# Performance work log

Measured on AMD Instinct MI355X. Metric: run time of the kernel, lower is better.

Reference implementation:

```python
import jax, jax.numpy as jnp
import numpy as np

L, B, S, D, N, H = 4, 4, 1024, 1024, 64, 16   # layers, batch, seq, d_model, d_state, heads
DI = 2 * D      # d_inner (expand_factor=2)
DH = D // H     # head dim
DF = 4 * D      # ffn hidden
SCALE = 1.0 / np.sqrt(DH)


def setup_inputs() -> dict:
    key = jax.random.key(0)
    ks = jax.random.split(key, 12)
    w = lambda k, sh: jax.random.normal(k, sh, jnp.float32) * 0.02
    return {
        "x": jax.random.normal(ks[0], (B, S, D), jnp.float32),
        "A_log": jax.random.normal(ks[1], (L, N), jnp.float32),
        "Dp": jax.random.normal(ks[2], (L, D), jnp.float32),
        "W_in": w(ks[3], (L, 2 * DI, D)), "b_in": jnp.zeros((L, 2 * DI), jnp.float32),
        "W_xp": w(ks[4], (L, N, DI)), "b_xp": jnp.zeros((L, N), jnp.float32),
        "W_dt": w(ks[5], (L, D, DI)), "b_dt": jnp.zeros((L, D), jnp.float32),
        "W_out": w(ks[6], (L, D, DI)), "b_out": jnp.zeros((L, D), jnp.float32),
        "W_qkv": w(ks[7], (L, 3 * D, D)), "b_qkv": jnp.zeros((L, 3 * D), jnp.float32),
        "W_ao": w(ks[8], (L, D, D)), "b_ao": jnp.zeros((L, D), jnp.float32),
        "g1": jnp.ones((L, D), jnp.float32), "be1": jnp.zeros((L, D), jnp.float32),
        "g2": jnp.ones((L, D), jnp.float32), "be2": jnp.zeros((L, D), jnp.float32),
        "W_f1": w(ks[9], (L, DF, D)), "b_f1": jnp.zeros((L, DF), jnp.float32),
        "W_f2": w(ks[10], (L, D, DF)), "b_f2": jnp.zeros((L, D), jnp.float32),
    }


def _ln(x, g, b, eps=1e-5):
    mu = x.mean(-1, keepdims=True)
    var = ((x - mu) ** 2).mean(-1, keepdims=True)
    return (x - mu) * jax.lax.rsqrt(var + eps) * g + b


def _mamba(x, A_log, Dp, W_in, b_in, W_xp, b_xp, W_dt, b_dt, W_out, b_out):
    xr = jnp.einsum('bsd,od->bso', x, W_in) + b_in          # [b,s,2*DI]
    xi, res = jnp.split(xr, 2, axis=-1)
    xi = jax.nn.silu(xi)
    A = -jnp.exp(A_log)                                      # [N]
    delta = jax.nn.softplus(jnp.einsum('bsi,di->bsd', xi, W_dt) + b_dt)  # [b,s,D]
    m = delta.mean(-1)                                       # [b,s]
    A_disc = jnp.exp(A[None, None, :] * m[:, :, None])       # [b,s,N]
    u = jnp.einsum('bsi,ni->bsn', xi, W_xp) + b_xp           # [b,s,N]

    def step(state, inp):
        a_t, u_t = inp
        state = a_t * state + u_t                            # [b,N]
        return state, state.sum(-1)                          # carry, emit sum over d_state

    init = jnp.zeros((x.shape[0], A_log.shape[0]), x.dtype)
    _, ssum = jax.lax.scan(step, init, (A_disc.swapaxes(0, 1), u.swapaxes(0, 1)))
    ssum = ssum.swapaxes(0, 1)                               # [b,s]
    y = ssum[..., None] * xi                                 # [b,s,DI]
    y = y * jax.nn.silu(res)
    y = jnp.einsum('bsi,di->bsd', y, W_out) + b_out
    return y + x * Dp


def _attn(x, W_qkv, b_qkv, W_ao, b_ao):
    b, s, d = x.shape
    qkv = jnp.einsum('bsd,od->bso', x, W_qkv) + b_qkv        # [b,s,3d]
    qkv = qkv.reshape(b, s, 3, H, DH)
    q = jnp.moveaxis(qkv[:, :, 0], 2, 1)                     # [b,h,s,dh]
    k = jnp.moveaxis(qkv[:, :, 1], 2, 1)
    v = jnp.moveaxis(qkv[:, :, 2], 2, 1)
    scores = jnp.einsum('bhqd,bhkd->bhqk', q, k) * SCALE
    wts = jax.nn.softmax(scores, axis=-1)
    o = jnp.einsum('bhqk,bhkd->bhqd', wts, v)
    o = jnp.moveaxis(o, 1, 2).reshape(b, s, d)
    return jnp.einsum('bsd,od->bso', o, W_ao) + b_ao


def _forward(x, A_log, Dp, W_in, b_in, W_xp, b_xp, W_dt, b_dt, W_out, b_out,
             W_qkv, b_qkv, W_ao, b_ao, g1, be1, g2, be2, W_f1, b_f1, W_f2, b_f2):
    for l in range(L):
        m = _mamba(x, A_log[l], Dp[l], W_in[l], b_in[l], W_xp[l], b_xp[l],
                   W_dt[l], b_dt[l], W_out[l], b_out[l])
        x = _ln(x + m, g1[l], be1[l])
        a = _attn(x, W_qkv[l], b_qkv[l], W_ao[l], b_ao[l])
        x = _ln(x + a, g2[l], be2[l])
        h = jax.nn.gelu(jnp.einsum('bsd,fd->bsf', x, W_f1[l]) + b_f1[l], approximate=False)
        x = x + jnp.einsum('bsf,df->bsd', h, W_f2[l]) + b_f2[l]
    return x


def reference(x, A_log, Dp, W_in, b_in, W_xp, b_xp, W_dt, b_dt, W_out, b_out,
              W_qkv, b_qkv, W_ao, b_ao, g1, be1, g2, be2, W_f1, b_f1, W_f2, b_f2):
    return _forward(x, A_log, Dp, W_in, b_in, W_xp, b_xp, W_dt, b_dt, W_out, b_out,
                    W_qkv, b_qkv, W_ao, b_ao, g1, be1, g2, be2, W_f1, b_f1, W_f2, b_f2)
```

## Files before the change

### kernel.cpp

```cpp
#include <hip/hip_runtime.h>
#include <math.h>

typedef unsigned short ushort_t;
typedef unsigned int uint_t;
typedef __attribute__((ext_vector_type(8))) short short8;
typedef __attribute__((ext_vector_type(4))) float f32x4;

constexpr int Bb = 4, Ss = 1024, Dd = 1024, Nn = 64, Hh = 16;
constexpr int DIi = 2048, DFf = 4096;
constexpr int TOKENS = Bb * Ss;

constexpr size_t O_IN  = 0;
constexpr size_t O_DT  = 4194304;
constexpr size_t O_XP  = O_DT + 2097152;
constexpr size_t O_OUT = O_XP + 262144;
constexpr size_t O_QKV = O_OUT + 2097152;
constexpr size_t O_AO  = O_QKV + 3145728;
constexpr size_t O_F1  = O_AO + 1048576;
constexpr size_t O_F2  = O_F1 + 4194304;
constexpr size_t W_TOTAL = O_F2 + 4194304;
constexpr size_t W_QUADS = W_TOTAL / 4;

enum { EPI_SPLIT = 0, EPI_QKV, EPI_GELU, EPI_DTXP, EPI_DP, EPI_F32, EPI_RESID };

__device__ __forceinline__ float siluf(float x) { return x / (1.f + expf(-x)); }
__device__ __forceinline__ float softplusf(float x) { return fmaxf(x, 0.f) + log1pf(expf(-fabsf(x))); }
__device__ __forceinline__ float geluf(float x) { return 0.5f * x * (1.f + erff(x * 0.7071067811865476f)); }

__device__ __forceinline__ float bf2f(uint_t u) {
    union { uint_t i; float f; } v; v.i = u << 16; return v.f;
}
__device__ __forceinline__ ushort_t f2bf(float f) {
    union { float f; uint_t i; } v; v.f = f;
    return (ushort_t)((v.i + 0x7FFFu + ((v.i >> 16) & 1u)) >> 16);
}

__device__ __forceinline__ void gload_lds16(const ushort_t* g, ushort_t* l) {
    __builtin_amdgcn_global_load_lds(
        (const __attribute__((address_space(1))) unsigned int*)g,
        (__attribute__((address_space(3))) unsigned int*)l, 16, 0, 0);
}

__device__ __forceinline__ void wait_vm(int n) {
    if (n == 0)      asm volatile("s_waitcnt vmcnt(0)" ::: "memory");
    else if (n == 3) asm volatile("s_waitcnt vmcnt(3)" ::: "memory");
    else if (n == 4) asm volatile("s_waitcnt vmcnt(4)" ::: "memory");
    else if (n == 6) asm volatile("s_waitcnt vmcnt(6)" ::: "memory");
    else             asm volatile("s_waitcnt vmcnt(8)" ::: "memory");
}

template <int EPI>
__global__ __launch_bounds__(512) void gemm_mfma256(
    const ushort_t* __restrict__ A, const ushort_t* __restrict__ Bw,
    const float* __restrict__ bias, int M, int N, int K,
    ushort_t* __restrict__ ob0, ushort_t* __restrict__ ob1)
{
    constexpr int NBUF = 3, DEPTH = 2, L = 4;
    constexpr int BUFSZ = 16384;
    __shared__ __attribute__((aligned(16))) ushort_t AB[NBUF * BUFSZ];

    const int tid = threadIdx.x;
    const int lane = tid & 63, wid = tid >> 6;
    const int wr = wid >> 2, wc = wid & 3;
    const int l15 = lane & 15, lg = lane >> 4;

    int bx = blockIdx.x, by = blockIdx.y;
    const int gx = gridDim.x, gy = gridDim.y;
    if ((gy & 3) == 0 && (gx & 1) == 0) {
        const int s = by * gx + bx;
        const int xcd = s & 7, c = s >> 3;
        const int gyc = gy >> 2, gxc = gx >> 1;
        by = (xcd & 3) * gyc + (c % gyc);
        bx = (xcd >> 2) * gxc + (c / gyc);
    }
    const int m0 = by << 8, n0 = bx << 8;

    f32x4 acc[8][4];
#pragma unroll
    for (int i = 0; i < 8; ++i)
#pragma unroll
        for (int j = 0; j < 4; ++j) { acc[i][j][0]=0.f; acc[i][j][1]=0.f; acc[i][j][2]=0.f; acc[i][j][3]=0.f; }

    const int srow4 = lane >> 2;
    const int scc4  = (lane & 3) ^ ((lane >> 3) & 3);
    const ushort_t* Ag = A + (size_t)(m0 + wid * 32 + srow4) * K + scc4 * 8;
    const ushort_t* Bg = Bw + (size_t)(n0 + wid * 32 + srow4) * K + scc4 * 8;

    auto STAGE = [&](int b_, int k0_) {
        ushort_t* d_ = AB + b_ * BUFSZ;
        gload_lds16(Ag + k0_,                  d_ + (wid * 32) * 32);
        gload_lds16(Ag + (size_t)16 * K + k0_, d_ + (wid * 32 + 16) * 32);
        gload_lds16(Bg + k0_,                  d_ + 8192 + (wid * 32) * 32);
        gload_lds16(Bg + (size_t)16 * K + k0_, d_ + 8192 + (wid * 32 + 16) * 32);
    };

    const int NS = K >> 5;
    STAGE(0, 0);
    STAGE(1, 32);
    wait_vm(4);
    __builtin_amdgcn_s_barrier();

    const int chAB = (lg ^ ((l15 >> 1) & 3)) * 8;
    int bc = 0, bp = DEPTH;
    for (int s = 0; s < NS; ++s) {
        if (s + DEPTH < NS) STAGE(bp, (s + DEPTH) << 5);
        const ushort_t* As_ = AB + bc * BUFSZ;
        const ushort_t* Bs_ = As_ + 8192;
        short8 af[8], bfr[4];
#pragma unroll
        for (int mi = 0; mi < 8; ++mi)
            af[mi] = *(const short8*)&As_[(wr * 128 + mi * 16 + l15) * 32 + chAB];
#pragma unroll
        for (int nj = 0; nj < 4; ++nj)
            bfr[nj] = *(const short8*)&Bs_[(wc * 64 + nj * 16 + l15) * 32 + chAB];
#pragma unroll
        for (int mi = 0; mi < 8; ++mi)
#pragma unroll
            for (int nj = 0; nj < 4; ++nj)
                acc[mi][nj] = __builtin_amdgcn_mfma_f32_16x16x32_bf16(
                    af[mi], bfr[nj], acc[mi][nj], 0, 0, 0);
        if (s + 1 < NS) {
            wait_vm((s + 2 < NS) ? 4 : 0);
            __builtin_amdgcn_s_barrier();
        }
        bc = (bc + 1 == NBUF) ? 0 : bc + 1;
        bp = (bp + 1 == NBUF) ? 0 : bp + 1;
    }
    __syncthreads();

    const bool lo = (EPI != EPI_SPLIT) || (n0 < DIi);
#pragma unroll
    for (int pass = 0; pass < 2; ++pass) {
        if (pass) __syncthreads();
        if (wr == pass) {
#pragma unroll
            for (int nj = 0; nj < 4; ++nj) {
                const int coll = wc * 64 + nj * 16 + l15;
                const float bv = bias[n0 + coll];
#pragma unroll
                for (int mi = 0; mi < 8; ++mi)
#pragma unroll
                    for (int r = 0; r < 4; ++r) {
                        float v = acc[mi][nj][r] + bv;
                        if (EPI == EPI_SPLIT) v = lo ? siluf(v) : v;
                        else if (EPI == EPI_GELU) v = geluf(v);
                        AB[(mi * 16 + lg * 4 + r) * 256 + coll] = f2bf(v);
                    }
            }
        }
        __syncthreads();
        const int tok0 = m0 + pass * 128;
        if (EPI == EPI_QKV && n0 >= 2048) {
            const int bb = tok0 >> 10, srow0 = tok0 & 1023;
#pragma unroll
            for (int it = 0; it < 8; ++it) {
                const int task = it * 512 + tid;
                const int dim = task & 255;
                const int strip = task >> 8;
                uint_t w[4];
#pragma unroll
                for (int j = 0; j < 4; ++j) {
                    const int s2 = strip * 8 + 2 * j;
                    w[j] = (uint_t)AB[s2 * 256 + dim] | ((uint_t)AB[(s2 + 1) * 256 + dim] << 16);
                }
                const int vd = (n0 - 2048) + dim;
                *(uint4*)&ob1[((size_t)(bb * Hh + (vd >> 6)) * 64 + (vd & 63)) * Ss + srow0 + strip * 8] =
                    make_uint4(w[0], w[1], w[2], w[3]);
            }
        } else {
            ushort_t* dst = (EPI == EPI_SPLIT) ? (lo ? ob0 : ob1) : ob0;
            const int Nd = (EPI == EPI_SPLIT) ? DIi : N;
            const int nb = (EPI == EPI_SPLIT && !lo) ? (n0 - DIi) : n0;
#pragma unroll
            for (int it = 0; it < 8; ++it) {
                const int c = it * 512 + tid;
                const int row = c >> 5, ch = c & 31;
                *(uint4*)&dst[(size_t)(tok0 + row) * Nd + nb + ch * 8] =
                    *(const uint4*)&AB[row * 256 + ch * 8];
            }
        }
    }
}

template <int EPI, int MT, int NBUF, int XBY>
__global__ __launch_bounds__(256) void gemm_mfma(
    const ushort_t* __restrict__ A, const ushort_t* __restrict__ Bw,
    const float* __restrict__ bias, int M, int N, int K,
    float* __restrict__ of0, float* __restrict__ of1,
    ushort_t* __restrict__ ob0, ushort_t* __restrict__ ob1,
    const float* __restrict__ e0, const float* __restrict__ e1)
{
    constexpr int BUFSZ = (MT == 128) ? 8192 : 6144;
    constexpr int DEPTH = NBUF - 1;
    constexpr int L     = (MT == 128) ? 4 : 3;
    constexpr int NJ    = (MT == 128) ? 4 : 2;
    constexpr int XBX   = 8 / XBY;
    __shared__ __attribute__((aligned(16))) ushort_t AB[NBUF * BUFSZ];

    const int tid = threadIdx.x;
    const int lane = tid & 63, wid = tid >> 6;
    const int wr = (MT == 128) ? (wid >> 1) : 0;
    const int wc = (MT == 128) ? (wid & 1) : wid;
    const int l15 = lane & 15, lg = lane >> 4;

    int bx = blockIdx.x, by = blockIdx.y;
    const int gx = gridDim.x, gy = gridDim.y;
    if ((gy % XBY) == 0 && (gx % XBX) == 0) {
        const int s = by * gx + bx;
        const int xcd = s & 7, c = s >> 3;
        const int gyc = gy / XBY, gxc = gx / XBX;
        by = (xcd % XBY) * gyc + (c % gyc);
        bx = (xcd / XBY) * gxc + (c / gyc);
    }
    const int m0 = by * MT, n0 = bx << 7;

    f32x4 acc[4][NJ];
#pragma unroll
    for (int i = 0; i < 4; ++i)
#pragma unroll
        for (int j = 0; j < NJ; ++j) { acc[i][j][0] = 0.f; acc[i][j][1] = 0.f; acc[i][j][2] = 0.f; acc[i][j][3] = 0.f; }

    const int srow4 = lane >> 2;
    const int scc4  = (lane & 3) ^ ((lane >> 3) & 3);
    const ushort_t* Ag = A + (size_t)(m0 + wid * 32 + srow4) * K + scc4 * 8;
    const ushort_t* Bg = Bw + (size_t)(n0 + wid * 32 + srow4) * K + scc4 * 8;
    const ushort_t* sb64[3];
    int do64[3];
    if (MT == 64) {
#pragma unroll
        for (int j = 0; j < 3; ++j) {
            const int i = wid * 3 + j;
            const bool isA = i < 4;
            const int rb = (isA ? i : i - 4) * 16;
            sb64[j] = (isA ? A + (size_t)(m0 + rb + srow4) * K
                           : Bw + (size_t)(n0 + rb + srow4) * K) + scc4 * 8;
            do64[j] = (isA ? 0 : 2048) + rb * 32;
        }
    }

    auto STAGE = [&](int b_, int k0_) {
        ushort_t* d_ = AB + b_ * BUFSZ;
        if constexpr (MT == 128) {
            gload_lds16(Ag + k0_,                  d_ + (wid * 32) * 32);
            gload_lds16(Ag + (size_t)16 * K + k0_, d_ + (wid * 32 + 16) * 32);
            gload_lds16(Bg + k0_,                  d_ + 4096 + (wid * 32) * 32);
            gload_lds16(Bg + (size_t)16 * K + k0_, d_ + 4096 + (wid * 32 + 16) * 32);
        } else {
#pragma unroll
            for (int j = 0; j < 3; ++j)
                gload_lds16(sb64[j] + k0_, d_ + do64[j]);
        }
    };

    const int NS = K >> 5;
#pragma unroll
    for (int p = 0; p < DEPTH; ++p) STAGE(p, p * 32);
    wait_vm((DEPTH - 1) * L);
    __builtin_amdgcn_s_barrier();

    const int chAB = (lg ^ ((l15 >> 1) & 3)) * 8;
    int bc = 0, bp = DEPTH;
    for (int s = 0; s < NS; ++s) {
        if (s + DEPTH < NS) STAGE(bp, (s + DEPTH) << 5);
        const ushort_t* As_ = AB + bc * BUFSZ;
        const ushort_t* Bs_ = As_ + ((MT == 128) ? 4096 : 2048);
        short8 af[4], bfr[NJ];
#pragma unroll
        for (int mi = 0; mi < 4; ++mi)
            af[mi] = *(const short8*)&As_[(wr * 64 + mi * 16 + l15) * 32 + chAB];
#pragma unroll
        for (int nj = 0; nj < NJ; ++nj)
            bfr[nj] = *(const short8*)&Bs_[(wc * (MT == 128 ? 64 : 32) + nj * 16 + l15) * 32 + chAB];
#pragma unroll
        for (int mi = 0; mi < 4; ++mi)
#pragma unroll
            for (int nj = 0; nj < NJ; ++nj)
                acc[mi][nj] = __builtin_amdgcn_mfma_f32_16x16x32_bf16(
                    af[mi], bfr[nj], acc[mi][nj], 0, 0, 0);
        if (s + 1 < NS) {
            const int rem = NS - 2 - s;
            wait_vm(((rem < DEPTH - 1) ? rem : DEPTH - 1) * L);
            __builtin_amdgcn_s_barrier();
        }
        bc = (bc + 1 == NBUF) ? 0 : bc + 1;
        bp = (bp + 1 == NBUF) ? 0 : bp + 1;
    }
    __syncthreads();

    if constexpr (MT == 128) {
        const bool lo = true; (void)lo;
#pragma unroll
        for (int nj = 0; nj < 4; ++nj) {
            const int coll = wc * 64 + nj * 16 + l15;
            const float bv = bias[n0 + coll];
#pragma unroll
            for (int mi = 0; mi < 4; ++mi)
#pragma unroll
                for (int r = 0; r < 4; ++r)
                    AB[(wr * 64 + mi * 16 + lg * 4 + r) * 128 + coll] = f2bf(acc[mi][nj][r] + bv);
        }
        __syncthreads();
#pragma unroll
        for (int i = 0; i < 8; ++i) {
            const int c = i * 256 + tid;
            const int row = c >> 4, ch = c & 15;
            *(uint4*)&ob0[(size_t)(m0 + row) * N + n0 + ch * 8] =
                *(const uint4*)&AB[row * 128 + ch * 8];
        }
    } else {
        float* Cf = (float*)AB;
#pragma unroll
        for (int nj = 0; nj < NJ; ++nj) {
            const int coll = wc * 32 + nj * 16 + l15;
            const float bv = bias[n0 + coll];
#pragma unroll
            for (int mi = 0; mi < 4; ++mi)
#pragma unroll
                for (int r = 0; r < 4; ++r)
                    Cf[(mi * 16 + lg * 4 + r) * 128 + coll] = acc[mi][nj][r] + bv;
        }
        __syncthreads();
#pragma unroll
        for (int i = 0; i < 8; ++i) {
            const int c = i * 256 + tid;
            const int row = c >> 5, ch = c & 31;
            const int grow = m0 + row;
            const int gcol = n0 + ch * 4;
            float4 v = *(const float4*)&Cf[row * 128 + ch * 4];
            if (EPI == EPI_DTXP) {
                if (n0 < Dd) {
                    float ps = softplusf(v.x) + softplusf(v.y) + softplusf(v.z) + softplusf(v.w);
#pragma unroll
                    for (int off = 1; off < 32; off <<= 1) ps += __shfl_xor(ps, off);
                    if ((lane & 31) == 0)
                        of0[(size_t)grow * 8 + (n0 >> 7)] = ps;
                } else {
                    *(float4*)&of1[(size_t)grow * 128 + (gcol - Dd)] = v;
                }
            } else if (EPI == EPI_DP) {
                const float4 e = *(const float4*)&e0[(size_t)grow * N + gcol];
                const float4 d = *(const float4*)&e1[gcol];
                v.x = fmaf(e.x, d.x, v.x); v.y = fmaf(e.y, d.y, v.y);
                v.z = fmaf(e.z, d.z, v.z); v.w = fmaf(e.w, d.w, v.w);
                *(float4*)&of0[(size_t)grow * N + gcol] = v;
            } else if (EPI == EPI_F32) {
                *(float4*)&of0[(size_t)grow * N + gcol] = v;
            } else {
                const float4 e = *(const float4*)&e0[(size_t)grow * N + gcol];
                v.x += e.x; v.y += e.y; v.z += e.z; v.w += e.w;
                *(float4*)&of0[(size_t)grow * N + gcol] = v;
                uint2 w;
                w.x = (uint_t)f2bf(v.x) | ((uint_t)f2bf(v.y) << 16);
                w.y = (uint_t)f2bf(v.z) | ((uint_t)f2bf(v.w) << 16);
                *(uint2*)&ob0[(size_t)grow * N + gcol] = w;
            }
        }
    }
}

__global__ __launch_bounds__(256) void convert_weights_kernel(
    const float* __restrict__ Win, const float* __restrict__ Wdt,
    const float* __restrict__ Wxp, const float* __restrict__ Wout,
    const float* __restrict__ Wqkv, const float* __restrict__ Wao,
    const float* __restrict__ Wf1, const float* __restrict__ Wf2,
    const float* __restrict__ bdt, const float* __restrict__ bxp,
    ushort_t* __restrict__ dst, float* __restrict__ bcat)
{
    size_t q = (size_t)blockIdx.x * blockDim.x + threadIdx.x;
    if (q < 288) {
#pragma unroll
        for (int j = 0; j < 4; ++j) {
            const int e = (int)q * 4 + j;
            bcat[e] = (e < Dd) ? bdt[e] : ((e < Dd + Nn) ? bxp[e - Dd] : 0.f);
        }
    }
    const size_t stride = (size_t)gridDim.x * blockDim.x;
    for (; q < W_QUADS; q += stride) {
        const size_t e = q * 4;
        float4 v;
        if (e < O_DT)       v = *(const float4*)&Win[e - O_IN];
        else if (e < O_XP)  v = *(const float4*)&Wdt[e - O_DT];
        else if (e < O_OUT) {
            const size_t li = e - O_XP;
            const int row = (int)(li >> 11), colq = (int)(li & 2047);
            v = (row < Nn) ? *(const float4*)&Wxp[(size_t)row * DIi + colq]
                           : make_float4(0.f, 0.f, 0.f, 0.f);
        }
        else if (e < O_QKV) v = *(const float4*)&Wout[e - O_OUT];
        else if (e < O_AO)  v = *(const float4*)&Wqkv[e - O_QKV];
        else if (e < O_F1)  v = *(const float4*)&Wao[e - O_AO];
        else if (e < O_F2)  v = *(const float4*)&Wf1[e - O_F1];
        else                v = *(const float4*)&Wf2[e - O_F2];
        uint2 w;
        w.x = (uint_t)f2bf(v.x) | ((uint_t)f2bf(v.y) << 16);
        w.y = (uint_t)f2bf(v.z) | ((uint_t)f2bf(v.w) << 16);
        *(uint2*)&dst[e] = w;
    }
}

__global__ __launch_bounds__(256) void cvt_f32_bf16_kernel(
    const float* __restrict__ in, ushort_t* __restrict__ out)
{
    const size_t i4 = (size_t)blockIdx.x * blockDim.x + threadIdx.x;
    const float4 v = *(const float4*)&in[i4 * 4];
    uint2 w;
    w.x = (uint_t)f2bf(v.x) | ((uint_t)f2bf(v.y) << 16);
    w.y = (uint_t)f2bf(v.z) | ((uint_t)f2bf(v.w) << 16);
    *(uint2*)&out[i4 * 4] = w;
}

__global__ __launch_bounds__(256) void ln_residual_kernel(
    float* __restrict__ xio, const float* __restrict__ addin,
    const float* __restrict__ g, const float* __restrict__ be,
    ushort_t* __restrict__ xb)
{
    __shared__ float red[8];
    const int tid = threadIdx.x;
    const size_t base = (size_t)blockIdx.x * Dd;
    const float4 xv = *(const float4*)&xio[base + tid * 4];
    const float4 av = *(const float4*)&addin[base + tid * 4];
    float v[4] = {xv.x + av.x, xv.y + av.y, xv.z + av.z, xv.w + av.w};
    float s = v[0] + v[1] + v[2] + v[3];
    float s2 = v[0] * v[0] + v[1] * v[1] + v[2] * v[2] + v[3] * v[3];
#pragma unroll
    for (int off = 32; off; off >>= 1) { s += __shfl_xor(s, off); s2 += __shfl_xor(s2, off); }
    if ((tid & 63) == 0) { red[tid >> 6] = s; red[4 + (tid >> 6)] = s2; }
    __syncthreads();
    const float mu = (red[0] + red[1] + red[2] + red[3]) * (1.f / (float)Dd);
    const float var = (red[4] + red[5] + red[6] + red[7]) * (1.f / (float)Dd) - mu * mu;
    const float rstd = rsqrtf(var + 1e-5f);
    const float4 gv = *(const float4*)&g[tid * 4];
    const float4 bv = *(const float4*)&be[tid * 4];
    float o[4];
    o[0] = (v[0] - mu) * rstd * gv.x + bv.x;
    o[1] = (v[1] - mu) * rstd * gv.y + bv.y;
    o[2] = (v[2] - mu) * rstd * gv.z + bv.z;
    o[3] = (v[3] - mu) * rstd * gv.w + bv.w;
    *(float4*)&xio[base + tid * 4] = make_float4(o[0], o[1], o[2], o[3]);
    uint2 w;
    w.x = (uint_t)f2bf(o[0]) | ((uint_t)f2bf(o[1]) << 16);
    w.y = (uint_t)f2bf(o[2]) | ((uint_t)f2bf(o[3]) << 16);
    *(uint2*)&xb[base + tid * 4] = w;
}

__global__ __launch_bounds__(1024) void scan_fused_kernel(
    const float* __restrict__ A_log_l, const float* __restrict__ part,
    const float* __restrict__ u, float* __restrict__ ssum)
{
    __shared__ float Ps[16][64];
    __shared__ float Sl[16][64];
    __shared__ float Cs[16][64];
    __shared__ float Ms[16][64];
    const int b = blockIdx.x;
    const int tid = threadIdx.x;
    const int n = tid & 63, c = tid >> 6;
    const int t0 = b * Ss + c * 64;
    const float Aval = -expf(A_log_l[n]);

    {
        const float* pp = part + (size_t)(t0 + n) * 8;
        float ps = 0.f;
#pragma unroll
        for (int j = 0; j < 8; ++j) ps += pp[j];
        Ms[c][n] = ps * (1.f / 1024.f);
    }
    __syncthreads();

    float S = 0.f, msum = 0.f;
#pragma unroll 8
    for (int t = 0; t < 64; ++t) {
        const float mt = Ms[c][t];
        msum += mt;
        S = fmaf(expf(Aval * mt), S, u[(size_t)(t0 + t) * 128 + n]);
    }
    Ps[c][n] = expf(Aval * msum);
    Sl[c][n] = S;
    __syncthreads();

    if (c == 0) {
        float carry = 0.f;
#pragma unroll
        for (int cc = 0; cc < 16; ++cc) {
            Cs[cc][n] = carry;
            carry = fmaf(Ps[cc][n], carry, Sl[cc][n]);
        }
    }
    __syncthreads();

    float st = Cs[c][n];
#pragma unroll 4
    for (int t = 0; t < 64; ++t) {
        st = fmaf(expf(Aval * Ms[c][t]), st, u[(size_t)(t0 + t) * 128 + n]);
        float r = st;
#pragma unroll
        for (int off = 32; off; off >>= 1) r += __shfl_xor(r, off);
        if (n == 0) ssum[t0 + t] = r;
    }
}

__global__ __launch_bounds__(256) void y_gate_kernel(
    ushort_t* __restrict__ xi, const ushort_t* __restrict__ res,
    const float* __restrict__ ssum)
{
    const size_t i8 = (size_t)blockIdx.x * blockDim.x + threadIdx.x;
    const int t = (int)(i8 >> 8);
    const float sv = ssum[t];
    uint4 xw = *(const uint4*)&xi[i8 * 8];
    const uint4 rw = *(const uint4*)&res[i8 * 8];
    const uint_t xs[4] = {xw.x, xw.y, xw.z, xw.w};
    const uint_t rs[4] = {rw.x, rw.y, rw.z, rw.w};
    uint_t os[4];
#pragma unroll
    for (int j = 0; j < 4; ++j) {
        const float x0 = bf2f(xs[j] & 0xffffu), x1 = bf2f(xs[j] >> 16);
        const float r0 = bf2f(rs[j] & 0xffffu), r1 = bf2f(rs[j] >> 16);
        os[j] = (uint_t)f2bf(sv * x0 * siluf(r0)) | ((uint_t)f2bf(sv * x1 * siluf(r1)) << 16);
    }
    *(uint4*)&xi[i8 * 8] = make_uint4(os[0], os[1], os[2], os[3]);
}

__global__ __launch_bounds__(256) void attn_mfma_kernel(
    const ushort_t* __restrict__ qkv, const ushort_t* __restrict__ vt,
    ushort_t* __restrict__ out)
{
    __shared__ ushort_t Ks[64 * 64];
    __shared__ ushort_t Vs[64 * 64];
    __shared__ __attribute__((aligned(16))) ushort_t Pb[4][2560];

    const int tid = threadIdx.x;
    const int lane = tid & 63, wid = tid >> 6;
    const int b = blockIdx.z, h = blockIdx.y;
    const int q0 = blockIdx.x * 128 + wid * 32;
    const int l15 = lane & 15, lg = lane >> 4;
    constexpr float CEXP = 0.125f * 1.44269504f;

    short8 qf[2][2];
#pragma unroll
    for (int mi = 0; mi < 2; ++mi)
#pragma unroll
        for (int kk = 0; kk < 2; ++kk)
            qf[mi][kk] = *(const short8*)&qkv[(size_t)(b * Ss + q0 + mi * 16 + l15) * 3072
                                              + h * 64 + kk * 32 + lg * 8];

    f32x4 oacc[2][4];
#pragma unroll
    for (int mi = 0; mi < 2; ++mi)
#pragma unroll
        for (int nj = 0; nj < 4; ++nj) { oacc[mi][nj][0]=0.f; oacc[mi][nj][1]=0.f; oacc[mi][nj][2]=0.f; oacc[mi][nj][3]=0.f; }
    float lrun[2][4];
#pragma unroll
    for (int mi = 0; mi < 2; ++mi)
#pragma unroll
        for (int r = 0; r < 4; ++r) lrun[mi][r] = 0.f;

    const int srow = lane >> 3;
    const int scc  = (lane & 7) ^ srow;
    const ushort_t* Kg = qkv + (size_t)(b * Ss + wid * 16 + srow) * 3072 + 1024 + h * 64 + scc * 8;
    const ushort_t* Vg = vt + (size_t)((b * Hh + h) * 64 + wid * 16 + srow) * Ss + scc * 8;

    for (int kt = 0; kt < Ss / 64; ++kt) {
#pragma unroll
        for (int j = 0; j < 2; ++j) {
            gload_lds16(Kg + (size_t)(kt * 64 + j * 8) * 3072, Ks + (wid * 16 + j * 8) * 64);
            gload_lds16(Vg + (size_t)j * 8 * Ss + kt * 64,     Vs + (wid * 16 + j * 8) * 64);
        }
        __syncthreads();

        f32x4 sacc[2][4];
#pragma unroll
        for (int mi = 0; mi < 2; ++mi)
#pragma unroll
            for (int nj = 0; nj < 4; ++nj) { sacc[mi][nj][0]=0.f; sacc[mi][nj][1]=0.f; sacc[mi][nj][2]=0.f; sacc[mi][nj][3]=0.f; }
#pragma unroll
        for (int kk = 0; kk < 2; ++kk) {
            short8 kf[4];
#pragma unroll
            for (int nj = 0; nj < 4; ++nj) {
                const int row = nj * 16 + l15;
                const int ch = (kk * 4 + lg) ^ (row & 7);
                kf[nj] = *(const short8*)&Ks[row * 64 + ch * 8];
            }
#pragma unroll
            for (int mi = 0; mi < 2; ++mi)
#pragma unroll
                for (int nj = 0; nj < 4; ++nj)
                    sacc[mi][nj] = __builtin_amdgcn_mfma_f32_16x16x32_bf16(
                        qf[mi][kk], kf[nj], sacc[mi][nj], 0, 0, 0);
        }

#pragma unroll
        for (int mi = 0; mi < 2; ++mi)
#pragma unroll
            for (int nj = 0; nj < 4; ++nj) {
                const int bi = mi * 2 + (nj >> 1);
                const int chsw = ((nj & 1) * 2 + (l15 >> 3)) ^ lg;
#pragma unroll
                for (int r = 0; r < 4; ++r) {
                    const float p = exp2f(sacc[mi][nj][r] * CEXP);
                    lrun[mi][r] += p;
                    const int q15 = lg * 4 + r;
                    Pb[wid][bi * 640 + q15 * 40 + chsw * 8 + (lane & 7)] = f2bf(p);
                }
            }

#pragma unroll
        for (int kk = 0; kk < 2; ++kk) {
            short8 pa[2], vb[4];
#pragma unroll
            for (int mi = 0; mi < 2; ++mi) {
                const int chsw = lg ^ (l15 >> 2);
                pa[mi] = *(const short8*)&Pb[wid][(mi * 2 + kk) * 640 + l15 * 40 + chsw * 8];
            }
#pragma unroll
            for (int nj = 0; nj < 4; ++nj) {
                const int row = nj * 16 + l15;
                const int ch = (kk * 4 + lg) ^ (row & 7);
                vb[nj] = *(const short8*)&Vs[row * 64 + ch * 8];
            }
#pragma unroll
            for (int mi = 0; mi < 2; ++mi)
#pragma unroll
                for (int nj = 0; nj < 4; ++nj)
                    oacc[mi][nj] = __builtin_amdgcn_mfma_f32_16x16x32_bf16(
                        pa[mi], vb[nj], oacc[mi][nj], 0, 0, 0);
        }
        __syncthreads();
    }

#pragma unroll
    for (int mi = 0; mi < 2; ++mi)
#pragma unroll
        for (int r = 0; r < 4; ++r) {
            float s = lrun[mi][r];
#pragma unroll
            for (int off = 1; off < 16; off <<= 1) s += __shfl_xor(s, off);
            lrun[mi][r] = 1.f / s;
        }
#pragma unroll
    for (int mi = 0; mi < 2; ++mi)
#pragma unroll
        for (int r = 0; r < 4; ++r) {
            const int q = q0 + mi * 16 + lg * 4 + r;
            const float inv = lrun[mi][r];
#pragma unroll
            for (int nj = 0; nj < 4; ++nj)
                out[(size_t)(b * Ss + q) * Dd + h * 64 + nj * 16 + l15] =
                    f2bf(oacc[mi][nj][r] * inv);
        }
}

extern "C" void kernel_launch(void* const* d_in, const int* in_sizes, int n_in,
                              void* d_out, int out_size, void* d_ws, size_t ws_size,
                              hipStream_t stream)
{
    const float* x_in  = (const float*)d_in[0];
    const float* A_log = (const float*)d_in[1];
    const float* Dp    = (const float*)d_in[2];
    const float* W_in  = (const float*)d_in[3];
    const float* b_in  = (const float*)d_in[4];
    const float* W_xp  = (const float*)d_in[5];
    const float* b_xp  = (const float*)d_in[6];
    const float* W_dt  = (const float*)d_in[7];
    const float* b_dt  = (const float*)d_in[8];
    const float* W_out = (const float*)d_in[9];
    const float* b_out = (const float*)d_in[10];
    const float* W_qkv = (const float*)d_in[11];
    const float* b_qkv = (const float*)d_in[12];
    const float* W_ao  = (const float*)d_in[13];
    const float* b_ao  = (const float*)d_in[14];
    const float* g1    = (const float*)d_in[15];
    const float* be1   = (const float*)d_in[16];
    const float* g2    = (const float*)d_in[17];
    const float* be2   = (const float*)d_in[18];
    const float* W_f1  = (const float*)d_in[19];
    const float* b_f1  = (const float*)d_in[20];
    const float* W_f2  = (const float*)d_in[21];
    const float* b_f2  = (const float*)d_in[22];

    float* xf      = (float*)d_ws;
    float* a3      = xf + 4194304;
    float* ub      = a3 + 4194304;
    float* sb      = ub + 524288;
    float* part    = sb + 4096;
    float* bcat    = part + 32768;
    ushort_t* xb    = (ushort_t*)(bcat + 1152);
    ushort_t* xi_b  = xb + 4194304;
    ushort_t* res_b = xi_b + 8388608;
    ushort_t* qh_b  = res_b + 8388608;
    ushort_t* ao_b  = qh_b + 16777216;
    ushort_t* Wb    = ao_b + 4194304;
    ushort_t* vt_b  = Wb + W_TOTAL;

    hipMemcpyAsync(xf, x_in, (size_t)TOKENS * Dd * sizeof(float),
                   hipMemcpyDeviceToDevice, stream);
    cvt_f32_bf16_kernel<<<dim3(4096), dim3(256), 0, stream>>>(x_in, xb);

    const dim3 blk(256), blk512(512);

    for (int l = 0; l < 4; ++l) {
        convert_weights_kernel<<<dim3(2048), blk, 0, stream>>>(
            W_in + (size_t)l * 4194304, W_dt + (size_t)l * 2097152,
            W_xp + (size_t)l * 131072,  W_out + (size_t)l * 2097152,
            W_qkv + (size_t)l * 3145728, W_ao + (size_t)l * 1048576,
            W_f1 + (size_t)l * 4194304, W_f2 + (size_t)l * 4194304,
            b_dt + (size_t)l * 1024, b_xp + (size_t)l * Nn, Wb, bcat);

        gemm_mfma256<EPI_SPLIT><<<dim3(16, 16), blk512, 0, stream>>>(
            xb, Wb + O_IN, b_in + (size_t)l * 4096, TOKENS, 4096, 1024,
            xi_b, res_b);
        gemm_mfma<EPI_DTXP, 64, 4, 8><<<dim3(9, 64), blk, 0, stream>>>(
            xi_b, Wb + O_DT, bcat, TOKENS, 1152, 2048,
            part, ub, nullptr, nullptr, nullptr, nullptr);
        scan_fused_kernel<<<dim3(Bb), dim3(1024), 0, stream>>>(
            A_log + (size_t)l * Nn, part, ub, sb);
        y_gate_kernel<<<dim3(4096), blk, 0, stream>>>(xi_b, res_b, sb);
        gemm_mfma<EPI_DP, 64, 4, 8><<<dim3(8, 64), blk, 0, stream>>>(
            xi_b, Wb + O_OUT, b_out + (size_t)l * 1024, TOKENS, 1024, 2048,
            a3, nullptr, nullptr, nullptr, xf, Dp + (size_t)l * 1024);
        ln_residual_kernel<<<dim3(TOKENS), blk, 0, stream>>>(
            xf, a3, g1 + (size_t)l * 1024, be1 + (size_t)l * 1024, xb);
        gemm_mfma256<EPI_QKV><<<dim3(12, 16), blk512, 0, stream>>>(
            xb, Wb + O_QKV, b_qkv + (size_t)l * 3072, TOKENS, 3072, 1024,
            qh_b, vt_b);
        attn_mfma_kernel<<<dim3(8, Hh, Bb), blk, 0, stream>>>(qh_b, vt_b, ao_b);
        gemm_mfma<EPI_F32, 64, 4, 8><<<dim3(8, 64), blk, 0, stream>>>(
            ao_b, Wb + O_AO, b_ao + (size_t)l * 1024, TOKENS, 1024, 1024,
            a3, nullptr, nullptr, nullptr, nullptr, nullptr);
        ln_residual_kernel<<<dim3(TOKENS), blk, 0, stream>>>(
            xf, a3, g2 + (size_t)l * 1024, be2 + (size_t)l * 1024, xb);
        gemm_mfma256<EPI_GELU><<<dim3(16, 16), blk512, 0, stream>>>(
            xb, Wb + O_F1, b_f1 + (size_t)l * 4096, TOKENS, 4096, 1024,
            qh_b, nullptr);
        gemm_mfma<EPI_RESID, 64, 4, 8><<<dim3(8, 64), blk, 0, stream>>>(
            qh_b, Wb + O_F2, b_f2 + (size_t)l * 1024, TOKENS, 1024, 4096,
            xf, nullptr, xb, nullptr, xf, nullptr);
    }

    hipMemcpyAsync(d_out, xf, (size_t)TOKENS * Dd * sizeof(float),
                   hipMemcpyDeviceToDevice, stream);
    (void)in_sizes; (void)n_in; (void)out_size; (void)ws_size;
}
```

Measured before the change: 1.864 ms.

## Rework 256-wide GEMM to K=64 double buffering; move QKV to 128-tile GEMM

Rewrites the 256x256 GEMM kernel to stage K=64 slices with two buffers and an 8-way XOR swizzle. Each stage now issues eight LDS loads and waits for all of them before the barrier, and the two-pass epilogue becomes a single pass over a 128KB LDS tile. The QKV projection moves to the 128-tile templated GEMM, which gains the split, QKV-transpose and GELU epilogues. The 64-tile GEMMs go from 4 to 5 pipeline buffers. The aim is fewer barriers per K step and better occupancy, at the cost of a shallower prefetch (a full drain every stage) and heavy LDS use that may limit blocks per CU.

Result: faster. 1.781 ms (-4.5%).

```diff
diff --git a/kernel.cpp b/kernel.cpp
--- a/kernel.cpp
+++ b/kernel.cpp
@@ -46,19 +46,17 @@
     else if (n == 3) asm volatile("s_waitcnt vmcnt(3)" ::: "memory");
     else if (n == 4) asm volatile("s_waitcnt vmcnt(4)" ::: "memory");
     else if (n == 6) asm volatile("s_waitcnt vmcnt(6)" ::: "memory");
+    else if (n == 9) asm volatile("s_waitcnt vmcnt(9)" ::: "memory");
     else             asm volatile("s_waitcnt vmcnt(8)" ::: "memory");
 }
 
 template <int EPI>
-__global__ __launch_bounds__(512) void gemm_mfma256(
+__global__ __launch_bounds__(512, 2) void gemm_wide256(
     const ushort_t* __restrict__ A, const ushort_t* __restrict__ Bw,
     const float* __restrict__ bias, int M, int N, int K,
     ushort_t* __restrict__ ob0, ushort_t* __restrict__ ob1)
 {
-    constexpr int NBUF = 3, DEPTH = 2, L = 4;
-    constexpr int BUFSZ = 16384;
-    __shared__ __attribute__((aligned(16))) ushort_t AB[NBUF * BUFSZ];
-
+    __shared__ __attribute__((aligned(16))) ushort_t AB[65536];
     const int tid = threadIdx.x;
     const int lane = tid & 63, wid = tid >> 6;
     const int wr = wid >> 2, wc = wid & 3;
@@ -81,104 +79,84 @@
 #pragma unroll
         for (int j = 0; j < 4; ++j) { acc[i][j][0]=0.f; acc[i][j][1]=0.f; acc[i][j][2]=0.f; acc[i][j][3]=0.f; }
 
-    const int srow4 = lane >> 2;
-    const int scc4  = (lane & 3) ^ ((lane >> 3) & 3);
-    const ushort_t* Ag = A + (size_t)(m0 + wid * 32 + srow4) * K + scc4 * 8;
-    const ushort_t* Bg = Bw + (size_t)(n0 + wid * 32 + srow4) * K + scc4 * 8;
+    const int srow8 = lane >> 3;
+    const int scc8  = (lane & 7) ^ srow8;
+    const ushort_t* Ag = A + (size_t)(m0 + wid * 32 + srow8) * K + scc8 * 8;
+    const ushort_t* Bg = Bw + (size_t)(n0 + wid * 32 + srow8) * K + scc8 * 8;
 
     auto STAGE = [&](int b_, int k0_) {
-        ushort_t* d_ = AB + b_ * BUFSZ;
-        gload_lds16(Ag + k0_,                  d_ + (wid * 32) * 32);
-        gload_lds16(Ag + (size_t)16 * K + k0_, d_ + (wid * 32 + 16) * 32);
-        gload_lds16(Bg + k0_,                  d_ + 8192 + (wid * 32) * 32);
-        gload_lds16(Bg + (size_t)16 * K + k0_, d_ + 8192 + (wid * 32 + 16) * 32);
+        ushort_t* d_ = AB + b_ * 32768;
+#pragma unroll
+        for (int i = 0; i < 4; ++i) {
+            gload_lds16(Ag + (size_t)i * 8 * K + k0_, d_ + (wid * 32 + i * 8) * 64);
+            gload_lds16(Bg + (size_t)i * 8 * K + k0_, d_ + 16384 + (wid * 32 + i * 8) * 64);
+        }
     };
 
-    const int NS = K >> 5;
+    const int NS = K >> 6;
     STAGE(0, 0);
-    STAGE(1, 32);
-    wait_vm(4);
+    wait_vm(0);
     __builtin_amdgcn_s_barrier();
-
-    const int chAB = (lg ^ ((l15 >> 1) & 3)) * 8;
-    int bc = 0, bp = DEPTH;
+    int cur = 0;
     for (int s = 0; s < NS; ++s) {
-        if (s + DEPTH < NS) STAGE(bp, (s + DEPTH) << 5);
-        const ushort_t* As_ = AB + bc * BUFSZ;
-        const ushort_t* Bs_ = As_ + 8192;
-        short8 af[8], bfr[4];
+        if (s + 1 < NS) STAGE(cur ^ 1, (s + 1) << 6);
+        const ushort_t* As_ = AB + cur * 32768;
+        const ushort_t* Bs_ = As_ + 16384;
+#pragma unroll
+        for (int kk = 0; kk < 2; ++kk) {
+            short8 af[8], bfr[4];
+#pragma unroll
+            for (int mi = 0; mi < 8; ++mi) {
+                const int row = wr * 128 + mi * 16 + l15;
+                const int ch = (kk * 4 + lg) ^ (row & 7);
+                af[mi] = *(const short8*)&As_[row * 64 + ch * 8];
+            }
+#pragma unroll
+            for (int nj = 0; nj < 4; ++nj) {
+                const int row = wc * 64 + nj * 16 + l15;
+                const int ch = (kk * 4 + lg) ^ (row & 7);
+                bfr[nj] = *(const short8*)&Bs_[row * 64 + ch * 8];
+            }
+#pragma unroll
+            for (int mi = 0; mi < 8; ++mi)
+#pragma unroll
+                for (int nj = 0; nj < 4; ++nj)
+                    acc[mi][nj] = __builtin_amdgcn_mfma_f32_16x16x32_bf16(
+                        af[mi], bfr[nj], acc[mi][nj], 0, 0, 0);
+        }
+        if (s + 1 < NS) {
+            wait_vm(0);
+            __builtin_amdgcn_s_barrier();
+        }
+        cur ^= 1;
+    }
+    __syncthreads();
+
+    const bool lo = (EPI != EPI_SPLIT) || (n0 < DIi);
+#pragma unroll
+    for (int nj = 0; nj < 4; ++nj) {
+        const int coll = wc * 64 + nj * 16 + l15;
+        const float bv = bias[n0 + coll];
 #pragma unroll
         for (int mi = 0; mi < 8; ++mi)
-            af[mi] = *(const short8*)&As_[(wr * 128 + mi * 16 + l15) * 32 + chAB];
-#pragma unroll
-        for (int nj = 0; nj < 4; ++nj)
-            bfr[nj] = *(const short8*)&Bs_[(wc * 64 + nj * 16 + l15) * 32 + chAB];
-#pragma unroll
-        for (int mi = 0; mi < 8; ++mi)
-#pragma unroll
-            for (int nj = 0; nj < 4; ++nj)
-                acc[mi][nj] = __builtin_amdgcn_mfma_f32_16x16x32_bf16(
-                    af[mi], bfr[nj], acc[mi][nj], 0, 0, 0);
-        if (s + 1 < NS) {
-            wait_vm((s + 2 < NS) ? 4 : 0);
-            __builtin_amdgcn_s_barrier();
-        }
-        bc = (bc + 1 == NBUF) ? 0 : bc + 1;
-        bp = (bp + 1 == NBUF) ? 0 : bp + 1;
+#pragma unroll
+            for (int r = 0; r < 4; ++r) {
+                float v = acc[mi][nj][r] + bv;
+                if (EPI == EPI_SPLIT) v = lo ? siluf(v) : v;
+                else v = geluf(v);
+                AB[(wr * 128 + mi * 16 + lg * 4 + r) * 256 + coll] = f2bf(v);
+            }
     }
     __syncthreads();
-
-    const bool lo = (EPI != EPI_SPLIT) || (n0 < DIi);
-#pragma unroll
-    for (int pass = 0; pass < 2; ++pass) {
-        if (pass) __syncthreads();
-        if (wr == pass) {
-#pragma unroll
-            for (int nj = 0; nj < 4; ++nj) {
-                const int coll = wc * 64 + nj * 16 + l15;
-                const float bv = bias[n0 + coll];
-#pragma unroll
-                for (int mi = 0; mi < 8; ++mi)
-#pragma unroll
-                    for (int r = 0; r < 4; ++r) {
-                        float v = acc[mi][nj][r] + bv;
-                        if (EPI == EPI_SPLIT) v = lo ? siluf(v) : v;
-                        else if (EPI == EPI_GELU) v = geluf(v);
-                        AB[(mi * 16 + lg * 4 + r) * 256 + coll] = f2bf(v);
-                    }
-            }
-        }
-        __syncthreads();
-        const int tok0 = m0 + pass * 128;
-        if (EPI == EPI_QKV && n0 >= 2048) {
-            const int bb = tok0 >> 10, srow0 = tok0 & 1023;
-#pragma unroll
-            for (int it = 0; it < 8; ++it) {
-                const int task = it * 512 + tid;
-                const int dim = task & 255;
-                const int strip = task >> 8;
-                uint_t w[4];
-#pragma unroll
-                for (int j = 0; j < 4; ++j) {
-                    const int s2 = strip * 8 + 2 * j;
-                    w[j] = (uint_t)AB[s2 * 256 + dim] | ((uint_t)AB[(s2 + 1) * 256 + dim] << 16);
-                }
-                const int vd = (n0 - 2048) + dim;
-                *(uint4*)&ob1[((size_t)(bb * Hh + (vd >> 6)) * 64 + (vd & 63)) * Ss + srow0 + strip * 8] =
-                    make_uint4(w[0], w[1], w[2], w[3]);
-            }
-        } else {
-            ushort_t* dst = (EPI == EPI_SPLIT) ? (lo ? ob0 : ob1) : ob0;
-            const int Nd = (EPI == EPI_SPLIT) ? DIi : N;
-            const int nb = (EPI == EPI_SPLIT && !lo) ? (n0 - DIi) : n0;
-#pragma unroll
-            for (int it = 0; it < 8; ++it) {
-                const int c = it * 512 + tid;
-                const int row = c >> 5, ch = c & 31;
-                *(uint4*)&dst[(size_t)(tok0 + row) * Nd + nb + ch * 8] =
-                    *(const uint4*)&AB[row * 256 + ch * 8];
-            }
-        }
+    ushort_t* dst = (EPI == EPI_SPLIT) ? (lo ? ob0 : ob1) : ob0;
+    const int Nd = (EPI == EPI_SPLIT) ? DIi : N;
+    const int nb = (EPI == EPI_SPLIT && !lo) ? (n0 - DIi) : n0;
+#pragma unroll
+    for (int it = 0; it < 16; ++it) {
+        const int c = it * 512 + tid;
+        const int row = c >> 5, ch = c & 31;
+        *(uint4*)&dst[(size_t)(m0 + row) * Nd + nb + ch * 8] =
+            *(const uint4*)&AB[row * 256 + ch * 8];
     }
 }
 
@@ -288,7 +266,7 @@
     __syncthreads();
 
     if constexpr (MT == 128) {
-        const bool lo = true; (void)lo;
+        const bool lo = (EPI != EPI_SPLIT) || (n0 < DIi);
 #pragma unroll
         for (int nj = 0; nj < 4; ++nj) {
             const int coll = wc * 64 + nj * 16 + l15;
@@ -296,16 +274,42 @@
 #pragma unroll
             for (int mi = 0; mi < 4; ++mi)
 #pragma unroll
-                for (int r = 0; r < 4; ++r)
-                    AB[(wr * 64 + mi * 16 + lg * 4 + r) * 128 + coll] = f2bf(acc[mi][nj][r] + bv);
+                for (int r = 0; r < 4; ++r) {
+                    float v = acc[mi][nj][r] + bv;
+                    if (EPI == EPI_SPLIT) v = lo ? siluf(v) : v;
+                    else if (EPI == EPI_GELU) v = geluf(v);
+                    AB[(wr * 64 + mi * 16 + lg * 4 + r) * 128 + coll] = f2bf(v);
+                }
         }
         __syncthreads();
-#pragma unroll
-        for (int i = 0; i < 8; ++i) {
-            const int c = i * 256 + tid;
-            const int row = c >> 4, ch = c & 15;
-            *(uint4*)&ob0[(size_t)(m0 + row) * N + n0 + ch * 8] =
-                *(const uint4*)&AB[row * 128 + ch * 8];
+        if (EPI == EPI_QKV && n0 >= 2048) {
+            const int bb = m0 >> 10, srow0 = m0 & 1023;
+#pragma unroll
+            for (int it = 0; it < 8; ++it) {
+                const int task = it * 256 + tid;
+                const int dim = task & 127;
+                const int strip = task >> 7;
+                uint_t w[4];
+#pragma unroll
+                for (int j = 0; j < 4; ++j) {
+                    const int s2 = strip * 8 + 2 * j;
+                    w[j] = (uint_t)AB[s2 * 128 + dim] | ((uint_t)AB[(s2 + 1) * 128 + dim] << 16);
+                }
+                const int vd = (n0 - 2048) + dim;
+                *(uint4*)&ob1[((size_t)(bb * Hh + (vd >> 6)) * 64 + (vd & 63)) * Ss + srow0 + strip * 8] =
+                    make_uint4(w[0], w[1], w[2], w[3]);
+            }
+        } else {
+            ushort_t* dst = (EPI == EPI_SPLIT) ? (lo ? ob0 : ob1) : ob0;
+            const int Nd = (EPI == EPI_SPLIT) ? DIi : N;
+            const int nb = (EPI == EPI_SPLIT && !lo) ? (n0 - DIi) : n0;
+#pragma unroll
+            for (int i = 0; i < 8; ++i) {
+                const int c = i * 256 + tid;
+                const int row = c >> 4, ch = c & 15;
+                *(uint4*)&dst[(size_t)(m0 + row) * Nd + nb + ch * 8] =
+                    *(const uint4*)&AB[row * 128 + ch * 8];
+            }
         }
     } else {
         float* Cf = (float*)AB;
@@ -705,33 +709,33 @@
             W_f1 + (size_t)l * 4194304, W_f2 + (size_t)l * 4194304,
             b_dt + (size_t)l * 1024, b_xp + (size_t)l * Nn, Wb, bcat);
 
-        gemm_mfma256<EPI_SPLIT><<<dim3(16, 16), blk512, 0, stream>>>(
+        gemm_wide256<EPI_SPLIT><<<dim3(16, 16), blk512, 0, stream>>>(
             xb, Wb + O_IN, b_in + (size_t)l * 4096, TOKENS, 4096, 1024,
             xi_b, res_b);
-        gemm_mfma<EPI_DTXP, 64, 4, 8><<<dim3(9, 64), blk, 0, stream>>>(
+        gemm_mfma<EPI_DTXP, 64, 5, 8><<<dim3(9, 64), blk, 0, stream>>>(
             xi_b, Wb + O_DT, bcat, TOKENS, 1152, 2048,
             part, ub, nullptr, nullptr, nullptr, nullptr);
         scan_fused_kernel<<<dim3(Bb), dim3(1024), 0, stream>>>(
             A_log + (size_t)l * Nn, part, ub, sb);
         y_gate_kernel<<<dim3(4096), blk, 0, stream>>>(xi_b, res_b, sb);
-        gemm_mfma<EPI_DP, 64, 4, 8><<<dim3(8, 64), blk, 0, stream>>>(
+        gemm_mfma<EPI_DP, 64, 5, 8><<<dim3(8, 64), blk, 0, stream>>>(
             xi_b, Wb + O_OUT, b_out + (size_t)l * 1024, TOKENS, 1024, 2048,
             a3, nullptr, nullptr, nullptr, xf, Dp + (size_t)l * 1024);
         ln_residual_kernel<<<dim3(TOKENS), blk, 0, stream>>>(
             xf, a3, g1 + (size_t)l * 1024, be1 + (size_t)l * 1024, xb);
-        gemm_mfma256<EPI_QKV><<<dim3(12, 16), blk512, 0, stream>>>(
+        gemm_mfma<EPI_QKV, 128, 3, 4><<<dim3(24, 32), blk, 0, stream>>>(
             xb, Wb + O_QKV, b_qkv + (size_t)l * 3072, TOKENS, 3072, 1024,
-            qh_b, vt_b);
+            nullptr, nullptr, qh_b, vt_b, nullptr, nullptr);
         attn_mfma_kernel<<<dim3(8, Hh, Bb), blk, 0, stream>>>(qh_b, vt_b, ao_b);
-        gemm_mfma<EPI_F32, 64, 4, 8><<<dim3(8, 64), blk, 0, stream>>>(
+        gemm_mfma<EPI_F32, 64, 5, 8><<<dim3(8, 64), blk, 0, stream>>>(
             ao_b, Wb + O_AO, b_ao + (size_t)l * 1024, TOKENS, 1024, 1024,
             a3, nullptr, nullptr, nullptr, nullptr, nullptr);
         ln_residual_kernel<<<dim3(TOKENS), blk, 0, stream>>>(
             xf, a3, g2 + (size_t)l * 1024, be2 + (size_t)l * 1024, xb);
-        gemm_mfma256<EPI_GELU><<<dim3(16, 16), blk512, 0, stream>>>(
+        gemm_wide256<EPI_GELU><<<dim3(16, 16), blk512, 0, stream>>>(
             xb, Wb + O_F1, b_f1 + (size_t)l * 4096, TOKENS, 4096, 1024,
             qh_b, nullptr);
-        gemm_mfma<EPI_RESID, 64, 4, 8><<<dim3(8, 64), blk, 0, stream>>>(
+        gemm_mfma<EPI_RESID, 64, 5, 8><<<dim3(8, 64), blk, 0, stream>>>(
             qh_b, Wb + O_F2, b_f2 + (size_t)l * 1024, TOKENS, 1024, 4096,
             xf, nullptr, xb, nullptr, xf, nullptr);
     }
```
